# Optimization experiments

Measured on AMD Instinct MI355X. Metric: run time of the kernel, lower is better.

The kernel has to match this reference:

```python
import math
import jax, jax.numpy as jnp
import numpy as np

N_FFT = 1024
HOP = 320
WIN = 800
SR = 32000
N_MELS = 128
FMIN = 0.0
FMAX = SR / 2.0
NUM_BINS = N_FFT // 2 + 1  # 513
PREEMPH = 0.97


def _hann_window(n):
    # torch.hann_window(n, periodic=False): 0.5 - 0.5*cos(2*pi*i/(n-1))
    i = np.arange(n, dtype=np.float64)
    return (0.5 - 0.5 * np.cos(2.0 * np.pi * i / (n - 1))).astype(np.float32)


def _fourier_basis():
    offset = (N_FFT - WIN) // 2
    win_full = np.zeros(N_FFT, dtype=np.float64)
    win_full[offset:offset + WIN] = _hann_window(WIN)
    n = np.arange(N_FFT, dtype=np.float64)[None, :]
    k = np.arange(NUM_BINS, dtype=np.float64)[:, None]
    ang = 2.0 * np.pi * k * (n / float(N_FFT))
    cos_k = np.cos(ang) * win_full
    sin_k = -np.sin(ang) * win_full
    return np.concatenate([cos_k, sin_k], axis=0).astype(np.float32)  # [2*513, 1024]


def _kaldi_mel_banks():
    # torchaudio.compliance.kaldi.get_mel_banks with vtln_warp_factor=1.0
    num_fft_bins = N_FFT // 2
    fft_bin_width = SR / float(N_FFT)
    mel = lambda f: 1127.0 * np.log(1.0 + f / 700.0)
    mel_low, mel_high = mel(FMIN), mel(FMAX)
    delta = (mel_high - mel_low) / (N_MELS + 1)
    left = mel_low + np.arange(N_MELS, dtype=np.float64) * delta  # [M]
    right = left + 2.0 * delta
    freqs = fft_bin_width * np.arange(num_fft_bins, dtype=np.float64)
    m = mel(freqs)[None, :]  # [1, 512]
    up = (m - left[:, None]) / delta
    down = (right[:, None] - m) / delta
    bank = np.maximum(0.0, np.minimum(up, down))  # [128, 512]
    bank = np.pad(bank, ((0, 0), (0, 1)))  # pad one zero column -> [128, 513]
    return bank.astype(np.float32)


def setup_inputs() -> dict:
    key = jax.random.key(0)
    x = jax.random.normal(key, (32, 320000), dtype=jnp.float32)
    return {
        "x": x,
        "fourier_basis": jnp.asarray(_fourier_basis()),
        "mel_basis": jnp.asarray(_kaldi_mel_banks()),
    }


def reference(x, fourier_basis, mel_basis):
    # preemphasis: conv1d with kernel [-0.97, 1.0] (cross-correlation)
    y = x[:, 1:] - PREEMPH * x[:, :-1]  # [B, T-1]
    # center pad by n_fft//2
    pad = N_FFT // 2
    y = jnp.pad(y, ((0, 0), (pad, pad)))
    Tp = y.shape[1]
    frames = (Tp - N_FFT) // HOP + 1
    # frame extraction: [B, frames, n_fft]
    idx = jnp.arange(frames)[:, None] * HOP + jnp.arange(N_FFT)[None, :]
    f = y[:, idx]
    # explicit DFT via dense matmul: [B, 2*num_bins, frames]
    spec = jnp.einsum('btn,cn->bct', f, fourier_basis)
    real = spec[:, :NUM_BINS, :]
    imag = spec[:, NUM_BINS:, :]
    power = real * real + imag * imag  # [B, num_bins, frames]
    mel = jnp.einsum('mf,bft->bmt', mel_basis, power)
    log_mel = (jnp.log(mel + 1e-05) + 4.5) / 5.0
    return log_mel
```

## Files before the change

### kernel.cpp

```cpp
#include <hip/hip_runtime.h>
#include <math.h>

typedef _Float16 half8 __attribute__((ext_vector_type(8)));
typedef float f32x4 __attribute__((ext_vector_type(4)));

constexpr int kNFFT    = 1024;
constexpr int kHop     = 320;
constexpr int kMels    = 128;
constexpr int kFrames  = 1000;
constexpr int kBatch   = 32;
constexpr int kXLen    = 320000;
constexpr int kYLen    = kXLen - 1;
constexpr int kYPad    = 328704;
constexpr int kYOff    = 512;
constexpr float kPre   = 0.97f;
constexpr int kPStride = 544;

constexpr size_t kYLvl     = (size_t)kBatch * kYPad;
constexpr size_t kFragLvl  = 64ull * 32 * 64 * 8;
constexpr size_t kFragOff  = 2 * kYLvl;
constexpr size_t kMelFrOff = kFragOff + 2 * kFragLvl;
constexpr size_t kMelFrSz  = 8ull * 17 * 64 * 8;
constexpr size_t kPowOff   = kMelFrOff + kMelFrSz;

__global__ void prep_y(const float* __restrict__ x, _Float16* __restrict__ yp) {
    int i = blockIdx.x * 256 + threadIdx.x;
    int e0 = i * 8;
    if (e0 >= kYPad) return;
    int b = blockIdx.y;
    const float* xb = x + (size_t)b * kXLen;
    int yi = e0 - kYOff;
    float v[8];
    if (yi >= 0 && yi <= kXLen - 9) {
        float4 A = *(const float4*)(xb + yi);
        float4 B = *(const float4*)(xb + yi + 4);
        float C = xb[yi + 8];
        v[0] = A.y - kPre * A.x;  v[1] = A.z - kPre * A.y;
        v[2] = A.w - kPre * A.z;  v[3] = B.x - kPre * A.w;
        v[4] = B.y - kPre * B.x;  v[5] = B.z - kPre * B.y;
        v[6] = B.w - kPre * B.z;  v[7] = C   - kPre * B.w;
    } else {
        #pragma unroll
        for (int j = 0; j < 8; ++j) {
            int g = yi + j;
            v[j] = (g >= 0 && g < kYLen) ? xb[g + 1] - kPre * xb[g] : 0.0f;
        }
    }
    half8 hv, mv;
    #pragma unroll
    for (int j = 0; j < 8; ++j) {
        _Float16 h = (_Float16)v[j];
        hv[j] = h;
        mv[j] = (_Float16)(v[j] - (float)h);
    }
    size_t idx = (size_t)b * kYPad + e0;
    *(half8*)(yp + idx) = hv;
    *(half8*)(yp + idx + kYLvl) = mv;
}

__global__ void prep_frags(const float* __restrict__ basis, _Float16* __restrict__ fr) {
    int id = blockIdx.x * 256 + threadIdx.x;
    int L  = id & 63;
    int ks = (id >> 6) & 31;
    int g  = id >> 11;
    int r  = 16 * g + (L & 15);
    int orig = (r <= 512) ? r : r + 1;
    const float* src = basis + (size_t)orig * kNFFT + 32 * ks + (L >> 4) * 8;
    _Float16* dst = fr + (size_t)id * 8;
    #pragma unroll
    for (int j = 0; j < 8; ++j) {
        float a = src[j];
        _Float16 h = (_Float16)a;
        _Float16 m = (_Float16)(a - (float)h);
        dst[j] = h;
        dst[j + kFragLvl] = m;
    }
}

__global__ void prep_melfr(const float* __restrict__ melb, _Float16* __restrict__ fr) {
    int id = blockIdx.x * 256 + threadIdx.x;
    if (id >= 8 * 17 * 64) return;
    int f = id / 1088;
    int rem = id - f * 1088;
    int ks = rem >> 6;
    int L = rem & 63;
    int m = 16 * f + (L & 15);
    int kb = 32 * ks + (L >> 4) * 8;
    _Float16* dst = fr + (size_t)id * 8;
    #pragma unroll
    for (int j = 0; j < 8; ++j) {
        int k = kb + j;
        dst[j] = (k < 513) ? (_Float16)melb[(size_t)m * 513 + k] : (_Float16)0.0f;
    }
}

__global__ __launch_bounds__(512, 4)
void stft_power(const _Float16* __restrict__ frags,
                const _Float16* __restrict__ ypad,
                _Float16* __restrict__ pw) {
    __shared__ __align__(16) _Float16 ash[2][16 * 512];
    const int tid  = threadIdx.x;
    const int w    = tid >> 6;
    const int lane = tid & 63;
    const int quad = lane >> 4;
    const int l16  = lane & 15;
    const int nt = blockIdx.x, g = blockIdx.y, b = blockIdx.z;
    const int t0 = nt * 256 + w * 32;
    const _Float16* yb0 = ypad + (size_t)b * kYPad;
    const _Float16* yb1 = yb0 + kYLvl;

    f32x4 acc[8][2] = {};

    auto stageA = [&](int ks, int pbuf) {
        #pragma unroll
        for (int c = 0; c < 2; ++c) {
            int slot = w + 8 * c;
            int f = slot & 7, lv = slot >> 3;
            int Gf = (f < 4) ? (4 * g + f) : (32 + 4 * g + (f - 4));
            const _Float16* gp = frags + (size_t)lv * kFragLvl
                               + ((size_t)(Gf * 32 + ks) * 64 + lane) * 8;
            __builtin_amdgcn_global_load_lds(
                (const __attribute__((address_space(1))) void*)gp,
                (__attribute__((address_space(3))) void*)&ash[pbuf][slot * 512],
                16, 0, 0);
        }
    };
    auto loadB = [&](int ks, half8* bh, half8* bm) {
        #pragma unroll
        for (int nf = 0; nf < 2; ++nf) {
            int off = (t0 + nf * 16 + l16) * kHop + ks * 32 + quad * 8;
            bh[nf] = *(const half8*)(yb0 + off);
            bm[nf] = *(const half8*)(yb1 + off);
        }
    };
    auto compute = [&](int pbuf, half8* bh, half8* bm) {
        #pragma unroll
        for (int f = 0; f < 8; ++f) {
            half8 afh = *(const half8*)&ash[pbuf][f * 512 + lane * 8];
            half8 afm = *(const half8*)&ash[pbuf][(8 + f) * 512 + lane * 8];
            #pragma unroll
            for (int nf = 0; nf < 2; ++nf) {
                f32x4 a = acc[f][nf];
                a = __builtin_amdgcn_mfma_f32_16x16x32_f16(afh, bh[nf], a, 0, 0, 0);
                a = __builtin_amdgcn_mfma_f32_16x16x32_f16(afm, bh[nf], a, 0, 0, 0);
                a = __builtin_amdgcn_mfma_f32_16x16x32_f16(afh, bm[nf], a, 0, 0, 0);
                acc[f][nf] = a;
            }
        }
    };

    half8 bhA[2], bmA[2], bhB[2], bmB[2];
    stageA(0, 0);
    loadB(0, bhA, bmA);
    for (int kss = 0; kss < 16; ++kss) {
        int ks = 2 * kss;
        __syncthreads();
        stageA(ks + 1, 1);
        loadB(ks + 1, bhB, bmB);
        compute(0, bhA, bmA);
        __syncthreads();
        if (ks + 2 < 32) {
            stageA(ks + 2, 0);
            loadB(ks + 2, bhA, bmA);
        }
        compute(1, bhB, bmB);
    }

    #pragma unroll
    for (int mf = 0; mf < 4; ++mf) {
        int b0 = 64 * g + 16 * mf + 4 * quad;
        #pragma unroll
        for (int nf = 0; nf < 2; ++nf) {
            int t = t0 + nf * 16 + l16;
            size_t row = ((size_t)((b << 10) + t)) * kPStride;
            struct alignas(8) h4 { _Float16 v[4]; } pp;
            #pragma unroll
            for (int r = 0; r < 4; ++r) {
                float pA = acc[mf][nf][r];
                float pB = acc[4 + mf][nf][r];
                float p2 = pA * pA + pB * pB;
                if (g == 0 && mf == 0 && quad == 0 && r == 0) {
                    p2 = pA * pA;
                    pw[row + 512] = (_Float16)(pB * pB);
                }
                pp.v[r] = (_Float16)p2;
            }
            *(decltype(pp)*)&pw[row + b0] = pp;
        }
    }
}

__global__ __launch_bounds__(256)
void mel_mfma(const _Float16* __restrict__ melfr, const _Float16* __restrict__ pw,
              float* __restrict__ out) {
    const int tid  = threadIdx.x;
    const int w    = tid >> 6;
    const int lane = tid & 63;
    const int quad = lane >> 4;
    const int l16  = lane & 15;
    const int nt = blockIdx.x, b = blockIdx.y;
    const int t = nt * 64 + w * 16 + l16;

    f32x4 acc[8] = {};
    const _Float16* prow = pw + ((size_t)((b << 10) + t)) * kPStride;
    for (int ks = 0; ks < 17; ++ks) {
        half8 bp = *(const half8*)(prow + 32 * ks + quad * 8);
        #pragma unroll
        for (int f = 0; f < 8; ++f) {
            half8 af = *(const half8*)(melfr + ((size_t)(f * 17 + ks) * 64 + lane) * 8);
            acc[f] = __builtin_amdgcn_mfma_f32_16x16x32_f16(af, bp, acc[f], 0, 0, 0);
        }
    }
    if (t < kFrames) {
        #pragma unroll
        for (int f = 0; f < 8; ++f) {
            #pragma unroll
            for (int r = 0; r < 4; ++r) {
                int m = 16 * f + 4 * quad + r;
                out[((size_t)(b * kMels + m)) * kFrames + t] =
                    (__logf(acc[f][r] + 1e-5f) + 4.5f) * 0.2f;
            }
        }
    }
}

extern "C" void kernel_launch(void* const* d_in, const int* in_sizes, int n_in,
                              void* d_out, int out_size, void* d_ws, size_t ws_size,
                              hipStream_t stream) {
    const float* x     = (const float*)d_in[0];
    const float* basis = (const float*)d_in[1];
    const float* melb  = (const float*)d_in[2];
    float* out = (float*)d_out;

    _Float16* ws    = (_Float16*)d_ws;
    _Float16* ypad  = ws;
    _Float16* frags = ws + kFragOff;
    _Float16* melfr = ws + kMelFrOff;
    _Float16* pw    = ws + kPowOff;

    prep_y<<<dim3(kYPad / 8 / 256 + 1, kBatch), 256, 0, stream>>>(x, ypad);
    prep_frags<<<dim3(131072 / 256), 256, 0, stream>>>(basis, frags);
    prep_melfr<<<dim3((8 * 17 * 64 + 255) / 256), 256, 0, stream>>>(melb, melfr);
    stft_power<<<dim3(4, 8, kBatch), 512, 0, stream>>>(frags, ypad, pw);
    mel_mfma<<<dim3(16, kBatch), 256, 0, stream>>>(melfr, pw, out);
}
```

Baseline: 296.5 us.

## Merge prep kernels, remap STFT block order, widen mel tiles

Merges the three preprocessing kernels into one launch that dispatches on block index. The STFT power kernel now runs on a 1D grid whose block indices are remapped, so concurrently scheduled blocks share frequency groups and batches differently, which changes cache locality across the chiplets. The mel kernel has each wave cover two 16-frame tiles, reusing each mel-basis fragment across two MFMAs and halving the grid. These reduce launch overhead and redundant loads, but the smaller mel grid lowers parallelism.

```diff
diff --git a/kernel.cpp b/kernel.cpp
--- a/kernel.cpp
+++ b/kernel.cpp
@@ -23,74 +23,85 @@
 constexpr size_t kMelFrSz  = 8ull * 17 * 64 * 8;
 constexpr size_t kPowOff   = kMelFrOff + kMelFrSz;
 
-__global__ void prep_y(const float* __restrict__ x, _Float16* __restrict__ yp) {
-    int i = blockIdx.x * 256 + threadIdx.x;
-    int e0 = i * 8;
-    if (e0 >= kYPad) return;
-    int b = blockIdx.y;
-    const float* xb = x + (size_t)b * kXLen;
-    int yi = e0 - kYOff;
-    float v[8];
-    if (yi >= 0 && yi <= kXLen - 9) {
-        float4 A = *(const float4*)(xb + yi);
-        float4 B = *(const float4*)(xb + yi + 4);
-        float C = xb[yi + 8];
-        v[0] = A.y - kPre * A.x;  v[1] = A.z - kPre * A.y;
-        v[2] = A.w - kPre * A.z;  v[3] = B.x - kPre * A.w;
-        v[4] = B.y - kPre * B.x;  v[5] = B.z - kPre * B.y;
-        v[6] = B.w - kPre * B.z;  v[7] = C   - kPre * B.w;
+constexpr int kYJobBlks   = (kYPad / 8 + 255) / 256;
+constexpr int kYJobTotal  = kYJobBlks * kBatch;
+constexpr int kFragBlks   = 131072 / 256;
+constexpr int kMelBlks    = (8 * 17 * 64) / 256;
+constexpr int kPrepGrid   = kYJobTotal + kFragBlks + kMelBlks;
+
+__global__ void prep_all(const float* __restrict__ x, const float* __restrict__ basis,
+                         const float* __restrict__ melb, _Float16* __restrict__ ws) {
+    _Float16* ypad  = ws;
+    _Float16* fr    = ws + kFragOff;
+    _Float16* melfr = ws + kMelFrOff;
+    const int bid = blockIdx.x;
+    const int tid = threadIdx.x;
+
+    if (bid < kYJobTotal) {
+        int b = bid / kYJobBlks;
+        int blk = bid - b * kYJobBlks;
+        int e0 = (blk * 256 + tid) * 8;
+        if (e0 >= kYPad) return;
+        const float* xb = x + (size_t)b * kXLen;
+        int yi = e0 - kYOff;
+        float v[8];
+        if (yi >= 0 && yi <= kXLen - 9) {
+            float4 A = *(const float4*)(xb + yi);
+            float4 B = *(const float4*)(xb + yi + 4);
+            float C = xb[yi + 8];
+            v[0] = A.y - kPre * A.x;  v[1] = A.z - kPre * A.y;
+            v[2] = A.w - kPre * A.z;  v[3] = B.x - kPre * A.w;
+            v[4] = B.y - kPre * B.x;  v[5] = B.z - kPre * B.y;
+            v[6] = B.w - kPre * B.z;  v[7] = C   - kPre * B.w;
+        } else {
+            #pragma unroll
+            for (int j = 0; j < 8; ++j) {
+                int g = yi + j;
+                v[j] = (g >= 0 && g < kYLen) ? xb[g + 1] - kPre * xb[g] : 0.0f;
+            }
+        }
+        half8 hv, mv;
+        #pragma unroll
+        for (int j = 0; j < 8; ++j) {
+            _Float16 h = (_Float16)v[j];
+            hv[j] = h;
+            mv[j] = (_Float16)(v[j] - (float)h);
+        }
+        size_t idx = (size_t)b * kYPad + e0;
+        *(half8*)(ypad + idx) = hv;
+        *(half8*)(ypad + idx + kYLvl) = mv;
+    } else if (bid < kYJobTotal + kFragBlks) {
+        int id = (bid - kYJobTotal) * 256 + tid;
+        int L  = id & 63;
+        int ks = (id >> 6) & 31;
+        int g  = id >> 11;
+        int r  = 16 * g + (L & 15);
+        int orig = (r <= 512) ? r : r + 1;
+        const float* src = basis + (size_t)orig * kNFFT + 32 * ks + (L >> 4) * 8;
+        _Float16* dst = fr + (size_t)id * 8;
+        #pragma unroll
+        for (int j = 0; j < 8; ++j) {
+            float a = src[j];
+            _Float16 h = (_Float16)a;
+            _Float16 m = (_Float16)(a - (float)h);
+            dst[j] = h;
+            dst[j + kFragLvl] = m;
+        }
     } else {
+        int id = (bid - kYJobTotal - kFragBlks) * 256 + tid;
+        if (id >= 8 * 17 * 64) return;
+        int f = id / 1088;
+        int rem = id - f * 1088;
+        int ks = rem >> 6;
+        int L = rem & 63;
+        int m = 16 * f + (L & 15);
+        int kb = 32 * ks + (L >> 4) * 8;
+        _Float16* dst = melfr + (size_t)id * 8;
         #pragma unroll
         for (int j = 0; j < 8; ++j) {
-            int g = yi + j;
-            v[j] = (g >= 0 && g < kYLen) ? xb[g + 1] - kPre * xb[g] : 0.0f;
-        }
-    }
-    half8 hv, mv;
-    #pragma unroll
-    for (int j = 0; j < 8; ++j) {
-        _Float16 h = (_Float16)v[j];
-        hv[j] = h;
-        mv[j] = (_Float16)(v[j] - (float)h);
-    }
-    size_t idx = (size_t)b * kYPad + e0;
-    *(half8*)(yp + idx) = hv;
-    *(half8*)(yp + idx + kYLvl) = mv;
-}
-
-__global__ void prep_frags(const float* __restrict__ basis, _Float16* __restrict__ fr) {
-    int id = blockIdx.x * 256 + threadIdx.x;
-    int L  = id & 63;
-    int ks = (id >> 6) & 31;
-    int g  = id >> 11;
-    int r  = 16 * g + (L & 15);
-    int orig = (r <= 512) ? r : r + 1;
-    const float* src = basis + (size_t)orig * kNFFT + 32 * ks + (L >> 4) * 8;
-    _Float16* dst = fr + (size_t)id * 8;
-    #pragma unroll
-    for (int j = 0; j < 8; ++j) {
-        float a = src[j];
-        _Float16 h = (_Float16)a;
-        _Float16 m = (_Float16)(a - (float)h);
-        dst[j] = h;
-        dst[j + kFragLvl] = m;
-    }
-}
-
-__global__ void prep_melfr(const float* __restrict__ melb, _Float16* __restrict__ fr) {
-    int id = blockIdx.x * 256 + threadIdx.x;
-    if (id >= 8 * 17 * 64) return;
-    int f = id / 1088;
-    int rem = id - f * 1088;
-    int ks = rem >> 6;
-    int L = rem & 63;
-    int m = 16 * f + (L & 15);
-    int kb = 32 * ks + (L >> 4) * 8;
-    _Float16* dst = fr + (size_t)id * 8;
-    #pragma unroll
-    for (int j = 0; j < 8; ++j) {
-        int k = kb + j;
-        dst[j] = (k < 513) ? (_Float16)melb[(size_t)m * 513 + k] : (_Float16)0.0f;
+            int k = kb + j;
+            dst[j] = (k < 513) ? (_Float16)melb[(size_t)m * 513 + k] : (_Float16)0.0f;
+        }
     }
 }
 
@@ -104,7 +115,16 @@
     const int lane = tid & 63;
     const int quad = lane >> 4;
     const int l16  = lane & 15;
-    const int nt = blockIdx.x, g = blockIdx.y, b = blockIdx.z;
+
+    const int lin = blockIdx.x;
+    const int r_  = lin & 7;
+    const int j_  = lin >> 3;
+    const int g   = j_ & 7;
+    const int s_  = j_ >> 3;
+    const int pair = r_ * 16 + s_;
+    const int b   = pair >> 2;
+    const int nt  = pair & 3;
+
     const int t0 = nt * 256 + w * 32;
     const _Float16* yb0 = ypad + (size_t)b * kYPad;
     const _Float16* yb1 = yb0 + kYLvl;
@@ -175,15 +195,15 @@
             size_t row = ((size_t)((b << 10) + t)) * kPStride;
             struct alignas(8) h4 { _Float16 v[4]; } pp;
             #pragma unroll
-            for (int r = 0; r < 4; ++r) {
-                float pA = acc[mf][nf][r];
-                float pB = acc[4 + mf][nf][r];
+            for (int rr = 0; rr < 4; ++rr) {
+                float pA = acc[mf][nf][rr];
+                float pB = acc[4 + mf][nf][rr];
                 float p2 = pA * pA + pB * pB;
-                if (g == 0 && mf == 0 && quad == 0 && r == 0) {
+                if (g == 0 && mf == 0 && quad == 0 && rr == 0) {
                     p2 = pA * pA;
                     pw[row + 512] = (_Float16)(pB * pB);
                 }
-                pp.v[r] = (_Float16)p2;
+                pp.v[rr] = (_Float16)p2;
             }
             *(decltype(pp)*)&pw[row + b0] = pp;
         }
@@ -199,26 +219,37 @@
     const int quad = lane >> 4;
     const int l16  = lane & 15;
     const int nt = blockIdx.x, b = blockIdx.y;
-    const int t = nt * 64 + w * 16 + l16;
-
-    f32x4 acc[8] = {};
-    const _Float16* prow = pw + ((size_t)((b << 10) + t)) * kPStride;
+    const int t0 = nt * 128 + w * 32;
+
+    f32x4 acc[8][2] = {};
     for (int ks = 0; ks < 17; ++ks) {
-        half8 bp = *(const half8*)(prow + 32 * ks + quad * 8);
+        half8 bp[2];
+        #pragma unroll
+        for (int nf = 0; nf < 2; ++nf) {
+            int t = t0 + nf * 16 + l16;
+            bp[nf] = *(const half8*)(pw + ((size_t)((b << 10) + t)) * kPStride
+                                     + 32 * ks + quad * 8);
+        }
         #pragma unroll
         for (int f = 0; f < 8; ++f) {
             half8 af = *(const half8*)(melfr + ((size_t)(f * 17 + ks) * 64 + lane) * 8);
-            acc[f] = __builtin_amdgcn_mfma_f32_16x16x32_f16(af, bp, acc[f], 0, 0, 0);
-        }
-    }
-    if (t < kFrames) {
-        #pragma unroll
-        for (int f = 0; f < 8; ++f) {
-            #pragma unroll
-            for (int r = 0; r < 4; ++r) {
-                int m = 16 * f + 4 * quad + r;
-                out[((size_t)(b * kMels + m)) * kFrames + t] =
-                    (__logf(acc[f][r] + 1e-5f) + 4.5f) * 0.2f;
+            #pragma unroll
+            for (int nf = 0; nf < 2; ++nf)
+                acc[f][nf] = __builtin_amdgcn_mfma_f32_16x16x32_f16(af, bp[nf], acc[f][nf], 0, 0, 0);
+        }
+    }
+    #pragma unroll
+    for (int f = 0; f < 8; ++f) {
+        #pragma unroll
+        for (int nf = 0; nf < 2; ++nf) {
+            int t = t0 + nf * 16 + l16;
+            if (t < kFrames) {
+                #pragma unroll
+                for (int r = 0; r < 4; ++r) {
+                    int m = 16 * f + 4 * quad + r;
+                    out[((size_t)(b * kMels + m)) * kFrames + t] =
+                        (__logf(acc[f][nf][r] + 1e-5f) + 4.5f) * 0.2f;
+                }
             }
         }
     }
@@ -233,14 +264,11 @@
     float* out = (float*)d_out;
 
     _Float16* ws    = (_Float16*)d_ws;
-    _Float16* ypad  = ws;
     _Float16* frags = ws + kFragOff;
     _Float16* melfr = ws + kMelFrOff;
     _Float16* pw    = ws + kPowOff;
 
-    prep_y<<<dim3(kYPad / 8 / 256 + 1, kBatch), 256, 0, stream>>>(x, ypad);
-    prep_frags<<<dim3(131072 / 256), 256, 0, stream>>>(basis, frags);
-    prep_melfr<<<dim3((8 * 17 * 64 + 255) / 256), 256, 0, stream>>>(melb, melfr);
-    stft_power<<<dim3(4, 8, kBatch), 512, 0, stream>>>(frags, ypad, pw);
-    mel_mfma<<<dim3(16, kBatch), 256, 0, stream>>>(melfr, pw, out);
-}
+    prep_all<<<dim3(kPrepGrid), 256, 0, stream>>>(x, basis, melb, ws);
+    stft_power<<<dim3(1024), 512, 0, stream>>>(frags, ws, pw);
+    mel_mfma<<<dim3(8, kBatch), 256, 0, stream>>>(melfr, pw, out);
+}
```

Result: no change. 297.9 us (+0.5%).
